# Kernel tuning notes

Measured on AMD Instinct MI355X. Metric: run time of the kernel, lower is better.

## Reference

```python
import jax, jax.numpy as jnp
import numpy as np
import math

DIM = 1024
HEADS = 16
HEAD_DIM = DIM // HEADS
FFN = 4096
B, S = 2, 2048
EPS = 1e-12


def layernorm(x, w, b):
    u = jnp.mean(x, axis=-1, keepdims=True)
    s = jnp.mean((x - u) ** 2, axis=-1, keepdims=True)
    return w * ((x - u) / jnp.sqrt(s + EPS)) + b


def setup_inputs() -> dict:
    key = jax.random.key(0)
    ks = jax.random.split(key, 8)
    scale = 0.02
    return {
        "x": jax.random.normal(ks[0], (B, S, DIM), dtype=jnp.float32),
        "mask": jnp.zeros((1, 1, S, S), dtype=jnp.float32),
        "wq": jax.random.normal(ks[1], (DIM, DIM), dtype=jnp.float32) * scale,
        "wk": jax.random.normal(ks[2], (DIM, DIM), dtype=jnp.float32) * scale,
        "wv": jax.random.normal(ks[3], (DIM, DIM), dtype=jnp.float32) * scale,
        "wo": jax.random.normal(ks[4], (DIM, DIM), dtype=jnp.float32) * scale,
        "w1": jax.random.normal(ks[5], (DIM, FFN), dtype=jnp.float32) * scale,
        "w2": jax.random.normal(ks[6], (FFN, DIM), dtype=jnp.float32) * scale,
        "ln1_w": jnp.ones((DIM,), dtype=jnp.float32),
        "ln1_b": jnp.zeros((DIM,), dtype=jnp.float32),
        "ln2_w": jnp.ones((DIM,), dtype=jnp.float32),
        "ln2_b": jnp.zeros((DIM,), dtype=jnp.float32),
    }


def reference(x, mask, wq, wk, wv, wo, w1, w2, ln1_w, ln1_b, ln2_w, ln2_b):
    # --- attention sub-block (pre-LN) ---
    h = layernorm(x, ln1_w, ln1_b)
    q = (h @ wq).reshape(B, S, HEADS, HEAD_DIM).transpose(0, 2, 1, 3)  # [B,H,S,D]
    k = (h @ wk).reshape(B, S, HEADS, HEAD_DIM).transpose(0, 2, 1, 3)
    v = (h @ wv).reshape(B, S, HEADS, HEAD_DIM).transpose(0, 2, 1, 3)
    scores = jnp.einsum("bhsd,bhtd->bhst", q, k) / math.sqrt(HEAD_DIM)
    scores = scores + mask
    probs = jax.nn.softmax(scores.astype(jnp.float32), axis=-1).astype(q.dtype)
    attn = jnp.einsum("bhst,bhtd->bhsd", probs, v)  # [B,H,S,D]
    attn = attn.transpose(0, 2, 1, 3).reshape(B, S, DIM)
    x = x + attn @ wo
    # --- FFN sub-block (pre-LN) ---
    h = layernorm(x, ln2_w, ln2_b)
    m = jax.nn.gelu(h @ w1, approximate=False) @ w2
    return x + m
```

## Files before the change

kernel.cpp:

```cpp
#include <hip/hip_runtime.h>
#include <math.h>


#define DIMSZ 1024
#define SEQ   2048
#define BATCH 2
#define NHEAD 16
#define HD    64
#define FFNSZ 4096
#define ROWS  (BATCH*SEQ)
#define KSPLIT 2
#define KRANGE (SEQ/KSPLIT)

typedef __attribute__((ext_vector_type(8))) short bf8_t;
typedef __attribute__((ext_vector_type(4))) float f4_t;

__device__ __forceinline__ unsigned short f2bf(float f) {
  union { float f; unsigned u; } c; c.f = f;
  unsigned u = c.u;
  return (unsigned short)((u + 0x7fffu + ((u >> 16) & 1u)) >> 16);
}

__device__ __forceinline__ float bf2f(unsigned short u) {
  union { unsigned u; float f; } c; c.u = ((unsigned)u) << 16; return c.f;
}

__device__ __forceinline__ float fast_exp2(float x) {
#if __has_builtin(__builtin_amdgcn_exp2f)
  return __builtin_amdgcn_exp2f(x);
#else
  return exp2f(x);
#endif
}

__device__ __forceinline__ unsigned int pk_trunc_bf16(float a, float b) {
#if __has_builtin(__builtin_amdgcn_perm)
  return __builtin_amdgcn_perm(__float_as_uint(b), __float_as_uint(a), 0x07060302u);
#else
  return (__float_as_uint(b) & 0xffff0000u) | (__float_as_uint(a) >> 16);
#endif
}

__device__ __forceinline__ void async16(const void* g, void* l) {
  __builtin_amdgcn_global_load_lds((const __attribute__((address_space(1))) void*)g,
                                   (__attribute__((address_space(3))) void*)l,
                                   16, 0, 0);
}

__device__ __forceinline__ f4_t mfma_bf16(bf8_t a, bf8_t b, f4_t c) {
  return __builtin_amdgcn_mfma_f32_16x16x32_bf16(a, b, c, 0, 0, 0);
}

__global__ __launch_bounds__(256) void ln_kernel(const float* __restrict__ x,
                                                 const float* __restrict__ w,
                                                 const float* __restrict__ b,
                                                 unsigned short* __restrict__ out) {
  int row  = blockIdx.x * 4 + (threadIdx.x >> 6);
  int lane = threadIdx.x & 63;
  const float4* xr = (const float4*)(x + (size_t)row * DIMSZ);
  float4 v[4];
  float s = 0.f, s2 = 0.f;
#pragma unroll
  for (int i = 0; i < 4; ++i) {
    v[i] = xr[lane + 64*i];
    s  += (v[i].x + v[i].y) + (v[i].z + v[i].w);
    s2 += (v[i].x*v[i].x + v[i].y*v[i].y) + (v[i].z*v[i].z + v[i].w*v[i].w);
  }
#pragma unroll
  for (int off = 32; off; off >>= 1) {
    s  += __shfl_xor(s,  off);
    s2 += __shfl_xor(s2, off);
  }
  float mean = s * (1.f/DIMSZ);
  float var  = s2 * (1.f/DIMSZ) - mean*mean;
  float rstd = rsqrtf(var + 1e-12f);
  const float4* wr = (const float4*)w;
  const float4* br = (const float4*)b;
#pragma unroll
  for (int i = 0; i < 4; ++i) {
    float4 wv = wr[lane + 64*i];
    float4 bv = br[lane + 64*i];
    ushort4 o;
    o.x = f2bf((v[i].x - mean) * rstd * wv.x + bv.x);
    o.y = f2bf((v[i].y - mean) * rstd * wv.y + bv.y);
    o.z = f2bf((v[i].z - mean) * rstd * wv.z + bv.z);
    o.w = f2bf((v[i].w - mean) * rstd * wv.w + bv.w);
    *(ushort4*)(out + (size_t)row * DIMSZ + (size_t)(lane + 64*i) * 4) = o;
  }
}

__global__ __launch_bounds__(256) void wtrans4_kernel(const float* __restrict__ w0,
                                                      const float* __restrict__ w1,
                                                      const float* __restrict__ w2,
                                                      const float* __restrict__ w3,
                                                      unsigned short* __restrict__ o0,
                                                      unsigned short* __restrict__ o1,
                                                      unsigned short* __restrict__ o2,
                                                      unsigned short* __restrict__ o3) {
  const int K = 1024, N = 1024;
  const float* w = (blockIdx.z == 0) ? w0 : (blockIdx.z == 1) ? w1 : (blockIdx.z == 2) ? w2 : w3;
  unsigned short* wT = (blockIdx.z == 0) ? o0 : (blockIdx.z == 1) ? o1 : (blockIdx.z == 2) ? o2 : o3;
  __shared__ float t[32][33];
  int tx = threadIdx.x & 31, ty = threadIdx.x >> 5;
  int n0 = blockIdx.x * 32, k0 = blockIdx.y * 32;
#pragma unroll
  for (int i = 0; i < 4; ++i)
    t[ty + 8*i][tx] = w[(size_t)(k0 + ty + 8*i) * N + n0 + tx];
  __syncthreads();
#pragma unroll
  for (int i = 0; i < 4; ++i)
    wT[(size_t)(n0 + ty + 8*i) * K + k0 + tx] = f2bf(t[tx][ty + 8*i]);
}

__global__ __launch_bounds__(256) void wtrans_kernel(const float* __restrict__ w,
                                                     unsigned short* __restrict__ wT,
                                                     int K, int N) {
  __shared__ float t[32][33];
  int tx = threadIdx.x & 31, ty = threadIdx.x >> 5;
  int n0 = blockIdx.x * 32, k0 = blockIdx.y * 32;
#pragma unroll
  for (int i = 0; i < 4; ++i)
    t[ty + 8*i][tx] = w[(size_t)(k0 + ty + 8*i) * N + n0 + tx];
  __syncthreads();
#pragma unroll
  for (int i = 0; i < 4; ++i)
    wT[(size_t)(n0 + ty + 8*i) * K + k0 + tx] = f2bf(t[tx][ty + 8*i]);
}

__global__ __launch_bounds__(256) void vt_kernel(const unsigned short* __restrict__ qkv,
                                                 unsigned short* __restrict__ vt) {
  __shared__ unsigned short tile[64][65];
  int bh = blockIdx.y, b = bh >> 4, h = bh & 15;
  int s0 = blockIdx.x * 64;
  int tx = threadIdx.x & 63, ty = threadIdx.x >> 6;
#pragma unroll
  for (int i = 0; i < 16; ++i) {
    int s = ty + i*4;
    tile[s][tx] = qkv[((size_t)(b*SEQ) + s0 + s) * 3072 + 2048 + h*HD + tx];
  }
  __syncthreads();
#pragma unroll
  for (int i = 0; i < 16; ++i) {
    int d = ty + i*4;
    vt[((size_t)bh * HD + d) * SEQ + s0 + tx] = tile[tx][d];
  }
}

template<int EPI, int NT>
__global__ __launch_bounds__(256) void gemm_bt(const unsigned short* __restrict__ A,
                                               const unsigned short* __restrict__ Bt,
                                               void* __restrict__ Cv,
                                               const float* __restrict__ res,
                                               int M, int N, int K) {
  constexpr int JT = NT / 32;
  __shared__ unsigned short As[2][128][32];
  __shared__ unsigned short Bs[2][NT][32];
  int tid  = threadIdx.x;
  int wv   = tid >> 6, lane = tid & 63, quad = lane >> 4, ml = lane & 15;
  int wrow = (wv >> 1) * 64, wcol = (wv & 1) * (NT/2);
  const unsigned short* Ab = A  + (size_t)blockIdx.y * 128 * K;
  const unsigned short* Bb = Bt + (size_t)blockIdx.x * NT  * K;

  f4_t acc[4][JT];
#pragma unroll
  for (int i = 0; i < 4; ++i)
#pragma unroll
    for (int j = 0; j < JT; ++j) acc[i][j] = (f4_t){0.f, 0.f, 0.f, 0.f};

  int r0 = tid >> 2, c0 = (tid & 3) * 8;

  for (int k0 = 0; k0 < K; k0 += 64) {
#pragma unroll
    for (int h = 0; h < 2; ++h) {
      const unsigned short* ap = Ab + (size_t)r0 * K + k0 + h*32 + c0;
      async16(ap,          &As[h][r0][c0]);
      async16(ap + 64*K,   &As[h][r0 + 64][c0]);
      const unsigned short* bp = Bb + (size_t)r0 * K + k0 + h*32 + c0;
      async16(bp,          &Bs[h][r0][c0]);
      if constexpr (NT == 128)
        async16(bp + 64*K, &Bs[h][r0 + 64][c0]);
    }
    __syncthreads();

#pragma unroll
    for (int h = 0; h < 2; ++h) {
      bf8_t af[4], bfr[JT];
#pragma unroll
      for (int i = 0; i < 4; ++i)
        af[i] = *(const bf8_t*)(&As[h][wrow + i*16 + ml][quad * 8]);
#pragma unroll
      for (int j = 0; j < JT; ++j)
        bfr[j] = *(const bf8_t*)(&Bs[h][wcol + j*16 + ml][quad * 8]);
#pragma unroll
      for (int i = 0; i < 4; ++i)
#pragma unroll
        for (int j = 0; j < JT; ++j)
          acc[i][j] = mfma_bf16(bfr[j], af[i], acc[i][j]);
    }
    __syncthreads();
  }

#pragma unroll
  for (int i = 0; i < 4; ++i) {
    int m = blockIdx.y * 128 + wrow + i*16 + ml;
#pragma unroll
    for (int j = 0; j < JT; ++j) {
      int n = blockIdx.x * NT + wcol + j*16 + quad*4;
      size_t off = (size_t)m * N + n;
      if constexpr (EPI == 2) {
        float4 rv = *(const float4*)(res + off);
        float4 ov;
        ov.x = rv.x + acc[i][j][0];
        ov.y = rv.y + acc[i][j][1];
        ov.z = rv.z + acc[i][j][2];
        ov.w = rv.w + acc[i][j][3];
        *(float4*)((float*)Cv + off) = ov;
      } else {
        float v0 = acc[i][j][0], v1 = acc[i][j][1], v2 = acc[i][j][2], v3 = acc[i][j][3];
        if constexpr (EPI == 1) {
          v0 = 0.5f * v0 * (1.f + erff(v0 * 0.70710678118654752f));
          v1 = 0.5f * v1 * (1.f + erff(v1 * 0.70710678118654752f));
          v2 = 0.5f * v2 * (1.f + erff(v2 * 0.70710678118654752f));
          v3 = 0.5f * v3 * (1.f + erff(v3 * 0.70710678118654752f));
        }
        ushort4 o;
        o.x = f2bf(v0); o.y = f2bf(v1); o.z = f2bf(v2); o.w = f2bf(v3);
        *(ushort4*)((unsigned short*)Cv + off) = o;
      }
    }
  }
}

__global__ __launch_bounds__(256) void attn_part(const unsigned short* __restrict__ qkv,
                                                 const unsigned short* __restrict__ vt,
                                                 const float* __restrict__ mask,
                                                 unsigned short* __restrict__ pbuf,
                                                 float* __restrict__ lbuf) {
  __shared__ unsigned short Ks[2][64][32];
  __shared__ unsigned short Vs[2][64][32];
  __shared__ unsigned short Ps[4][2][16][72];

  int kz = blockIdx.y;
  int bh = blockIdx.z, b = bh >> 4, h = bh & 15;
  int tid = threadIdx.x;
  int wv = tid >> 6, lane = tid & 63;
  int quad = lane >> 4, ml = lane & 15;
  int q0 = blockIdx.x * 128;
  int qA = q0 + wv * 32 + ml;
  int qB = qA + 16;
  int kbeg = kz * KRANGE;

  const unsigned short* qrowA = qkv + ((size_t)(b*SEQ) + qA) * 3072 + h*HD;
  const unsigned short* qrowB = qkv + ((size_t)(b*SEQ) + qB) * 3072 + h*HD;
  bf8_t qf[2][2];
  qf[0][0] = *(const bf8_t*)(qrowA + quad*8);
  qf[0][1] = *(const bf8_t*)(qrowA + 32 + quad*8);
  qf[1][0] = *(const bf8_t*)(qrowB + quad*8);
  qf[1][1] = *(const bf8_t*)(qrowB + 32 + quad*8);

  const unsigned short* kbase = qkv + ((size_t)(b*SEQ) + kbeg) * 3072 + DIMSZ + h*HD;
  const unsigned short* vbase = vt + (size_t)bh * HD * SEQ + kbeg;
  const float* mrowA = mask + (size_t)qA * SEQ + kbeg;
  const float* mrowB = mask + (size_t)qB * SEQ + kbeg;

  int srow = tid >> 2;
  int scol = (tid & 3) * 8;

  f4_t O[2][4];
#pragma unroll
  for (int g = 0; g < 2; ++g)
#pragma unroll
    for (int dt = 0; dt < 4; ++dt) O[g][dt] = (f4_t){0.f, 0.f, 0.f, 0.f};
  float lR[2] = {0.f, 0.f};

  const float C1 = 0.18033688011112042f;
  const float C2 = 1.4426950408889634f;

  for (int t0 = 0; t0 < KRANGE; t0 += 64) {
    float4 mvA[4], mvB[4];
#pragma unroll
    for (int mt = 0; mt < 4; ++mt) {
      mvA[mt] = *(const float4*)(mrowA + t0 + mt*16 + quad*4);
      mvB[mt] = *(const float4*)(mrowB + t0 + mt*16 + quad*4);
    }

    __syncthreads();
#pragma unroll
    for (int dh = 0; dh < 2; ++dh)
      async16(kbase + (size_t)(t0 + srow) * 3072 + dh*32 + scol,
              &Ks[dh][0][0] + (size_t)tid * 8);
#pragma unroll
    for (int kc = 0; kc < 2; ++kc)
      async16(vbase + (size_t)srow * SEQ + t0 + kc*32 + scol,
              &Vs[kc][0][0] + (size_t)tid * 8);
    __syncthreads();

#pragma unroll
    for (int mt = 0; mt < 4; ++mt) {
      bf8_t kf0 = *(const bf8_t*)(&Ks[0][mt*16 + ml][quad*8]);
      bf8_t kf1 = *(const bf8_t*)(&Ks[1][mt*16 + ml][quad*8]);
#pragma unroll
      for (int g = 0; g < 2; ++g) {
        f4_t s = (f4_t){0.f, 0.f, 0.f, 0.f};
        s = mfma_bf16(kf0, qf[g][0], s);
        s = mfma_bf16(kf1, qf[g][1], s);
        const float4& mv = g ? mvB[mt] : mvA[mt];
        float p0 = fast_exp2(fmaf(s[0], C1, mv.x * C2));
        float p1 = fast_exp2(fmaf(s[1], C1, mv.y * C2));
        float p2 = fast_exp2(fmaf(s[2], C1, mv.z * C2));
        float p3 = fast_exp2(fmaf(s[3], C1, mv.w * C2));
        lR[g] += (p0 + p1) + (p2 + p3);
        uint2 pk;
        pk.x = pk_trunc_bf16(p0, p1);
        pk.y = pk_trunc_bf16(p2, p3);
        *(uint2*)(&Ps[wv][g][ml][mt*16 + quad*4]) = pk;
      }
    }

#pragma unroll
    for (int kc = 0; kc < 2; ++kc) {
      bf8_t pfA = *(const bf8_t*)(&Ps[wv][0][ml][kc*32 + quad*8]);
      bf8_t pfB = *(const bf8_t*)(&Ps[wv][1][ml][kc*32 + quad*8]);
#pragma unroll
      for (int dt = 0; dt < 4; ++dt) {
        bf8_t vf = *(const bf8_t*)(&Vs[kc][dt*16 + ml][quad*8]);
        O[0][dt] = mfma_bf16(vf, pfA, O[0][dt]);
        O[1][dt] = mfma_bf16(vf, pfB, O[1][dt]);
      }
    }
  }

#pragma unroll
  for (int g = 0; g < 2; ++g) {
    lR[g] += __shfl_xor(lR[g], 16);
    lR[g] += __shfl_xor(lR[g], 32);
    int q = g ? qB : qA;
    size_t pb = ((size_t)(bh * KSPLIT + kz) * SEQ + q) * HD;
#pragma unroll
    for (int dt = 0; dt < 4; ++dt) {
      ushort4 o;
      o.x = f2bf(O[g][dt][0]);
      o.y = f2bf(O[g][dt][1]);
      o.z = f2bf(O[g][dt][2]);
      o.w = f2bf(O[g][dt][3]);
      *(ushort4*)(pbuf + pb + dt*16 + quad*4) = o;
    }
    if (quad == 0)
      lbuf[(size_t)(bh * KSPLIT + kz) * SEQ + q] = lR[g];
  }
}

__global__ __launch_bounds__(256) void attn_combine(const unsigned short* __restrict__ pbuf,
                                                    const float* __restrict__ lbuf,
                                                    unsigned short* __restrict__ attno) {
  int t = blockIdx.x * 256 + threadIdx.x;
  int dchunk = t & 15;
  int q = (t >> 4) & (SEQ - 1);
  int bh = t >> 15;
  int b = bh >> 4, h = bh & 15;
  size_t o0 = ((size_t)(bh * KSPLIT + 0) * SEQ + q) * HD + dchunk * 4;
  size_t o1 = ((size_t)(bh * KSPLIT + 1) * SEQ + q) * HD + dchunk * 4;
  ushort4 a = *(const ushort4*)(pbuf + o0);
  ushort4 c = *(const ushort4*)(pbuf + o1);
  float l = lbuf[(size_t)(bh * KSPLIT + 0) * SEQ + q]
          + lbuf[(size_t)(bh * KSPLIT + 1) * SEQ + q];
  float inv = 1.f / l;
  ushort4 o;
  o.x = f2bf((bf2f(a.x) + bf2f(c.x)) * inv);
  o.y = f2bf((bf2f(a.y) + bf2f(c.y)) * inv);
  o.z = f2bf((bf2f(a.z) + bf2f(c.z)) * inv);
  o.w = f2bf((bf2f(a.w) + bf2f(c.w)) * inv);
  *(ushort4*)(attno + ((size_t)(b*SEQ) + q) * DIMSZ + h*HD + dchunk*4) = o;
}

extern "C" void kernel_launch(void* const* d_in, const int* in_sizes, int n_in,
                              void* d_out, int out_size, void* d_ws, size_t ws_size,
                              hipStream_t stream) {
  const float* x    = (const float*)d_in[0];
  const float* mask = (const float*)d_in[1];
  const float* wq   = (const float*)d_in[2];
  const float* wk   = (const float*)d_in[3];
  const float* wvp  = (const float*)d_in[4];
  const float* wo   = (const float*)d_in[5];
  const float* w1   = (const float*)d_in[6];
  const float* w2   = (const float*)d_in[7];
  const float* ln1w = (const float*)d_in[8];
  const float* ln1b = (const float*)d_in[9];
  const float* ln2w = (const float*)d_in[10];
  const float* ln2b = (const float*)d_in[11];
  float* out = (float*)d_out;

  char* ws = (char*)d_ws;
  unsigned short* wqkvT  = (unsigned short*)(ws + 0);
  unsigned short* woT    = (unsigned short*)(ws + 6291456);
  unsigned short* w1T    = (unsigned short*)(ws + 8388608);
  unsigned short* w2T    = (unsigned short*)(ws + 16777216);
  unsigned short* attno  = (unsigned short*)(ws + 25165824);
  float*          x2     = (float*)         (ws + 33554432);
  unsigned short* hbuf   = (unsigned short*)(ws + 50331648);
  unsigned short* qkvb   = (unsigned short*)(ws + 58720256);
  unsigned short* vtb    = (unsigned short*)(ws + 83886080);
  unsigned short* gbuf   = (unsigned short*)(ws + 58720256);
  unsigned short* pbuf   = (unsigned short*)(ws + 33554432);
  float*          lbuf   = (float*)         (ws + 50331648);

  ln_kernel<<<ROWS/4, 256, 0, stream>>>(x, ln1w, ln1b, hbuf);
  wtrans4_kernel<<<dim3(32, 32, 4), 256, 0, stream>>>(wq, wk, wvp, wo,
      wqkvT, wqkvT + 1024*1024, wqkvT + 2*1024*1024, woT);
  wtrans_kernel<<<dim3(128, 32), 256, 0, stream>>>(w1, w1T, 1024, 4096);
  wtrans_kernel<<<dim3(32, 128), 256, 0, stream>>>(w2, w2T, 4096, 1024);
  gemm_bt<0,128><<<dim3(3072/128, 4096/128), 256, 0, stream>>>(hbuf, wqkvT, qkvb, nullptr, ROWS, 3072, 1024);
  vt_kernel<<<dim3(SEQ/64, BATCH*NHEAD), 256, 0, stream>>>(qkvb, vtb);
  attn_part<<<dim3(SEQ/128, KSPLIT, BATCH*NHEAD), 256, 0, stream>>>(qkvb, vtb, mask, pbuf, lbuf);
  attn_combine<<<(BATCH*NHEAD*SEQ*(HD/4))/256, 256, 0, stream>>>(pbuf, lbuf, attno);
  gemm_bt<2,64><<<dim3(1024/64, 4096/128), 256, 0, stream>>>(attno, woT, x2, x, ROWS, 1024, 1024);
  ln_kernel<<<ROWS/4, 256, 0, stream>>>(x2, ln2w, ln2b, hbuf);
  gemm_bt<1,128><<<dim3(4096/128, 4096/128), 256, 0, stream>>>(hbuf, w1T, gbuf, nullptr, ROWS, FFNSZ, 1024);
  gemm_bt<2,64><<<dim3(1024/64, 4096/128), 256, 0, stream>>>(gbuf, w2T, out, x2, ROWS, 1024, 4096);

  (void)in_sizes; (void)n_in; (void)out_size; (void)ws_size;
}
```

Measured before the change: 411.8 us.

## Fuse prep kernels, split-K the down-projection with atomics, use fast GELU

The first LayerNorm and all weight transposes are merged into a single prep launch, which removes three launches and lets the pieces overlap. The final FFN down-projection GEMM now uses a 4-way split-K. The second LayerNorm seeds the output with the residual, and each split atomically adds its partial sums into it, which gives more blocks for the K=4096 GEMM at the cost of atomic traffic and nondeterministic summation order. The erf-based GELU is replaced by the Abramowitz-Stegun polynomial using hardware rcp/exp2, which adds a small approximation error.

New measurement: 571.0 us. 1.39x slower.

```diff
diff --git a/kernel.cpp b/kernel.cpp
--- a/kernel.cpp
+++ b/kernel.cpp
@@ -33,6 +33,28 @@
 #endif
 }
 
+__device__ __forceinline__ float fast_rcp(float x) {
+#if __has_builtin(__builtin_amdgcn_rcpf)
+  return __builtin_amdgcn_rcpf(x);
+#else
+  return 1.f / x;
+#endif
+}
+
+__device__ __forceinline__ float gelu_fast(float x) {
+  float ax = fabsf(x) * 0.70710678118654752f;
+  float t  = fast_rcp(fmaf(0.3275911f, ax, 1.f));
+  float p  = fmaf(t, 1.061405429f, -1.453152027f);
+  p = fmaf(t, p, 1.421413741f);
+  p = fmaf(t, p, -0.284496736f);
+  p = fmaf(t, p, 0.254829592f);
+  p = p * t;
+  float e  = fast_exp2(-ax * ax * 1.4426950408889634f);
+  float er = fmaf(-p, e, 1.f);
+  er = copysignf(er, x);
+  return 0.5f * x * (1.f + er);
+}
+
 __device__ __forceinline__ unsigned int pk_trunc_bf16(float a, float b) {
 #if __has_builtin(__builtin_amdgcn_perm)
   return __builtin_amdgcn_perm(__float_as_uint(b), __float_as_uint(a), 0x07060302u);
@@ -51,10 +73,87 @@
   return __builtin_amdgcn_mfma_f32_16x16x32_bf16(a, b, c, 0, 0, 0);
 }
 
+__device__ __forceinline__ void atom_add_f32(float* p, float v) {
+  __hip_atomic_fetch_add(p, v, __ATOMIC_RELAXED, __HIP_MEMORY_SCOPE_AGENT);
+}
+
+__global__ __launch_bounds__(256) void prep_kernel(
+    const float* __restrict__ x,  const float* __restrict__ ln1w,
+    const float* __restrict__ ln1b, unsigned short* __restrict__ h1,
+    const float* __restrict__ wq, const float* __restrict__ wk,
+    const float* __restrict__ wv, const float* __restrict__ wo,
+    const float* __restrict__ w1, const float* __restrict__ w2,
+    unsigned short* __restrict__ wqkvT, unsigned short* __restrict__ woT,
+    unsigned short* __restrict__ w1T,   unsigned short* __restrict__ w2T) {
+  __shared__ float t[32][33];
+  int id = blockIdx.x;
+  if (id >= 12288) {
+    int row  = (id - 12288) * 4 + (threadIdx.x >> 6);
+    int lane = threadIdx.x & 63;
+    const float4* xr = (const float4*)(x + (size_t)row * DIMSZ);
+    float4 v[4];
+    float s = 0.f, s2 = 0.f;
+#pragma unroll
+    for (int i = 0; i < 4; ++i) {
+      v[i] = xr[lane + 64*i];
+      s  += (v[i].x + v[i].y) + (v[i].z + v[i].w);
+      s2 += (v[i].x*v[i].x + v[i].y*v[i].y) + (v[i].z*v[i].z + v[i].w*v[i].w);
+    }
+#pragma unroll
+    for (int off = 32; off; off >>= 1) {
+      s  += __shfl_xor(s,  off);
+      s2 += __shfl_xor(s2, off);
+    }
+    float mean = s * (1.f/DIMSZ);
+    float var  = s2 * (1.f/DIMSZ) - mean*mean;
+    float rstd = rsqrtf(var + 1e-12f);
+#pragma unroll
+    for (int i = 0; i < 4; ++i) {
+      float4 wv4 = ((const float4*)ln1w)[lane + 64*i];
+      float4 bv4 = ((const float4*)ln1b)[lane + 64*i];
+      ushort4 o;
+      o.x = f2bf((v[i].x - mean) * rstd * wv4.x + bv4.x);
+      o.y = f2bf((v[i].y - mean) * rstd * wv4.y + bv4.y);
+      o.z = f2bf((v[i].z - mean) * rstd * wv4.z + bv4.z);
+      o.w = f2bf((v[i].w - mean) * rstd * wv4.w + bv4.w);
+      *(ushort4*)(h1 + (size_t)row * DIMSZ + (size_t)(lane + 64*i) * 4) = o;
+    }
+    return;
+  }
+  const float* w; unsigned short* wT; int K, N, n0, k0;
+  if (id < 4096) {
+    int wsel = id >> 10, tt = id & 1023;
+    K = 1024; N = 1024;
+    n0 = (tt & 31) * 32; k0 = (tt >> 5) * 32;
+    w  = (wsel == 0) ? wq : (wsel == 1) ? wk : (wsel == 2) ? wv : wo;
+    wT = (wsel == 0) ? wqkvT : (wsel == 1) ? wqkvT + 1024*1024
+       : (wsel == 2) ? wqkvT + 2*1024*1024 : woT;
+  } else if (id < 8192) {
+    int tt = id - 4096;
+    K = 1024; N = 4096;
+    n0 = (tt & 127) * 32; k0 = (tt >> 7) * 32;
+    w = w1; wT = w1T;
+  } else {
+    int tt = id - 8192;
+    K = 4096; N = 1024;
+    n0 = (tt & 31) * 32; k0 = (tt >> 5) * 32;
+    w = w2; wT = w2T;
+  }
+  int tx = threadIdx.x & 31, ty = threadIdx.x >> 5;
+#pragma unroll
+  for (int i = 0; i < 4; ++i)
+    t[ty + 8*i][tx] = w[(size_t)(k0 + ty + 8*i) * N + n0 + tx];
+  __syncthreads();
+#pragma unroll
+  for (int i = 0; i < 4; ++i)
+    wT[(size_t)(n0 + ty + 8*i) * K + k0 + tx] = f2bf(t[tx][ty + 8*i]);
+}
+
 __global__ __launch_bounds__(256) void ln_kernel(const float* __restrict__ x,
                                                  const float* __restrict__ w,
                                                  const float* __restrict__ b,
-                                                 unsigned short* __restrict__ out) {
+                                                 unsigned short* __restrict__ out,
+                                                 float* __restrict__ cpy) {
   int row  = blockIdx.x * 4 + (threadIdx.x >> 6);
   int lane = threadIdx.x & 63;
   const float4* xr = (const float4*)(x + (size_t)row * DIMSZ);
@@ -74,57 +173,18 @@
   float mean = s * (1.f/DIMSZ);
   float var  = s2 * (1.f/DIMSZ) - mean*mean;
   float rstd = rsqrtf(var + 1e-12f);
-  const float4* wr = (const float4*)w;
-  const float4* br = (const float4*)b;
 #pragma unroll
   for (int i = 0; i < 4; ++i) {
-    float4 wv = wr[lane + 64*i];
-    float4 bv = br[lane + 64*i];
+    float4 wv = ((const float4*)w)[lane + 64*i];
+    float4 bv = ((const float4*)b)[lane + 64*i];
     ushort4 o;
     o.x = f2bf((v[i].x - mean) * rstd * wv.x + bv.x);
     o.y = f2bf((v[i].y - mean) * rstd * wv.y + bv.y);
     o.z = f2bf((v[i].z - mean) * rstd * wv.z + bv.z);
     o.w = f2bf((v[i].w - mean) * rstd * wv.w + bv.w);
     *(ushort4*)(out + (size_t)row * DIMSZ + (size_t)(lane + 64*i) * 4) = o;
-  }
-}
-
-__global__ __launch_bounds__(256) void wtrans4_kernel(const float* __restrict__ w0,
-                                                      const float* __restrict__ w1,
-                                                      const float* __restrict__ w2,
-                                                      const float* __restrict__ w3,
-                                                      unsigned short* __restrict__ o0,
-                                                      unsigned short* __restrict__ o1,
-                                                      unsigned short* __restrict__ o2,
-                                                      unsigned short* __restrict__ o3) {
-  const int K = 1024, N = 1024;
-  const float* w = (blockIdx.z == 0) ? w0 : (blockIdx.z == 1) ? w1 : (blockIdx.z == 2) ? w2 : w3;
-  unsigned short* wT = (blockIdx.z == 0) ? o0 : (blockIdx.z == 1) ? o1 : (blockIdx.z == 2) ? o2 : o3;
-  __shared__ float t[32][33];
-  int tx = threadIdx.x & 31, ty = threadIdx.x >> 5;
-  int n0 = blockIdx.x * 32, k0 = blockIdx.y * 32;
-#pragma unroll
-  for (int i = 0; i < 4; ++i)
-    t[ty + 8*i][tx] = w[(size_t)(k0 + ty + 8*i) * N + n0 + tx];
-  __syncthreads();
-#pragma unroll
-  for (int i = 0; i < 4; ++i)
-    wT[(size_t)(n0 + ty + 8*i) * K + k0 + tx] = f2bf(t[tx][ty + 8*i]);
-}
-
-__global__ __launch_bounds__(256) void wtrans_kernel(const float* __restrict__ w,
-                                                     unsigned short* __restrict__ wT,
-                                                     int K, int N) {
-  __shared__ float t[32][33];
-  int tx = threadIdx.x & 31, ty = threadIdx.x >> 5;
-  int n0 = blockIdx.x * 32, k0 = blockIdx.y * 32;
-#pragma unroll
-  for (int i = 0; i < 4; ++i)
-    t[ty + 8*i][tx] = w[(size_t)(k0 + ty + 8*i) * N + n0 + tx];
-  __syncthreads();
-#pragma unroll
-  for (int i = 0; i < 4; ++i)
-    wT[(size_t)(n0 + ty + 8*i) * K + k0 + tx] = f2bf(t[tx][ty + 8*i]);
+    if (cpy) ((float4*)(cpy + (size_t)row * DIMSZ))[lane + 64*i] = v[i];
+  }
 }
 
 __global__ __launch_bounds__(256) void vt_kernel(const unsigned short* __restrict__ qkv,
@@ -151,7 +211,7 @@
                                                const unsigned short* __restrict__ Bt,
                                                void* __restrict__ Cv,
                                                const float* __restrict__ res,
-                                               int M, int N, int K) {
+                                               int M, int N, int K, int klen) {
   constexpr int JT = NT / 32;
   __shared__ unsigned short As[2][128][32];
   __shared__ unsigned short Bs[2][NT][32];
@@ -160,6 +220,7 @@
   int wrow = (wv >> 1) * 64, wcol = (wv & 1) * (NT/2);
   const unsigned short* Ab = A  + (size_t)blockIdx.y * 128 * K;
   const unsigned short* Bb = Bt + (size_t)blockIdx.x * NT  * K;
+  int kbeg = blockIdx.z * klen;
 
   f4_t acc[4][JT];
 #pragma unroll
@@ -169,7 +230,7 @@
 
   int r0 = tid >> 2, c0 = (tid & 3) * 8;
 
-  for (int k0 = 0; k0 < K; k0 += 64) {
+  for (int k0 = kbeg; k0 < kbeg + klen; k0 += 64) {
 #pragma unroll
     for (int h = 0; h < 2; ++h) {
       const unsigned short* ap = Ab + (size_t)r0 * K + k0 + h*32 + c0;
@@ -215,13 +276,17 @@
         ov.z = rv.z + acc[i][j][2];
         ov.w = rv.w + acc[i][j][3];
         *(float4*)((float*)Cv + off) = ov;
+      } else if constexpr (EPI == 3) {
+        float* Co = (float*)Cv + off;
+        atom_add_f32(Co + 0, acc[i][j][0]);
+        atom_add_f32(Co + 1, acc[i][j][1]);
+        atom_add_f32(Co + 2, acc[i][j][2]);
+        atom_add_f32(Co + 3, acc[i][j][3]);
       } else {
         float v0 = acc[i][j][0], v1 = acc[i][j][1], v2 = acc[i][j][2], v3 = acc[i][j][3];
         if constexpr (EPI == 1) {
-          v0 = 0.5f * v0 * (1.f + erff(v0 * 0.70710678118654752f));
-          v1 = 0.5f * v1 * (1.f + erff(v1 * 0.70710678118654752f));
-          v2 = 0.5f * v2 * (1.f + erff(v2 * 0.70710678118654752f));
-          v3 = 0.5f * v3 * (1.f + erff(v3 * 0.70710678118654752f));
+          v0 = gelu_fast(v0); v1 = gelu_fast(v1);
+          v2 = gelu_fast(v2); v3 = gelu_fast(v3);
         }
         ushort4 o;
         o.x = f2bf(v0); o.y = f2bf(v1); o.z = f2bf(v2); o.w = f2bf(v3);
@@ -404,19 +469,17 @@
   unsigned short* pbuf   = (unsigned short*)(ws + 33554432);
   float*          lbuf   = (float*)         (ws + 50331648);
 
-  ln_kernel<<<ROWS/4, 256, 0, stream>>>(x, ln1w, ln1b, hbuf);
-  wtrans4_kernel<<<dim3(32, 32, 4), 256, 0, stream>>>(wq, wk, wvp, wo,
-      wqkvT, wqkvT + 1024*1024, wqkvT + 2*1024*1024, woT);
-  wtrans_kernel<<<dim3(128, 32), 256, 0, stream>>>(w1, w1T, 1024, 4096);
-  wtrans_kernel<<<dim3(32, 128), 256, 0, stream>>>(w2, w2T, 4096, 1024);
-  gemm_bt<0,128><<<dim3(3072/128, 4096/128), 256, 0, stream>>>(hbuf, wqkvT, qkvb, nullptr, ROWS, 3072, 1024);
+  prep_kernel<<<13312, 256, 0, stream>>>(x, ln1w, ln1b, hbuf,
+      wq, wk, wvp, wo, w1, w2,
+      wqkvT, woT, w1T, w2T);
+  gemm_bt<0,128><<<dim3(3072/128, 4096/128, 1), 256, 0, stream>>>(hbuf, wqkvT, qkvb, nullptr, ROWS, 3072, 1024, 1024);
   vt_kernel<<<dim3(SEQ/64, BATCH*NHEAD), 256, 0, stream>>>(qkvb, vtb);
   attn_part<<<dim3(SEQ/128, KSPLIT, BATCH*NHEAD), 256, 0, stream>>>(qkvb, vtb, mask, pbuf, lbuf);
   attn_combine<<<(BATCH*NHEAD*SEQ*(HD/4))/256, 256, 0, stream>>>(pbuf, lbuf, attno);
-  gemm_bt<2,64><<<dim3(1024/64, 4096/128), 256, 0, stream>>>(attno, woT, x2, x, ROWS, 1024, 1024);
-  ln_kernel<<<ROWS/4, 256, 0, stream>>>(x2, ln2w, ln2b, hbuf);
-  gemm_bt<1,128><<<dim3(4096/128, 4096/128), 256, 0, stream>>>(hbuf, w1T, gbuf, nullptr, ROWS, FFNSZ, 1024);
-  gemm_bt<2,64><<<dim3(1024/64, 4096/128), 256, 0, stream>>>(gbuf, w2T, out, x2, ROWS, 1024, 4096);
+  gemm_bt<2,64><<<dim3(1024/64, 4096/128, 1), 256, 0, stream>>>(attno, woT, x2, x, ROWS, 1024, 1024, 1024);
+  ln_kernel<<<ROWS/4, 256, 0, stream>>>(x2, ln2w, ln2b, hbuf, out);
+  gemm_bt<1,128><<<dim3(4096/128, 4096/128, 1), 256, 0, stream>>>(hbuf, w1T, gbuf, nullptr, ROWS, FFNSZ, 1024, 1024);
+  gemm_bt<3,64><<<dim3(1024/64, 4096/128, 4), 256, 0, stream>>>(gbuf, w2T, out, nullptr, ROWS, 1024, 4096, 1024);
 
   (void)in_sizes; (void)n_in; (void)out_size; (void)ws_size;
 }
```
